# Optimization experiments

Measured on AMD Instinct MI355X. Metric: run time of the kernel, lower is better.

The kernel has to match this reference:

```python
import jax, jax.numpy as jnp
import numpy as np

B, S, D = 2, 2048, 1024
H = 16
HD = D // H  # 64


def setup_inputs() -> dict:
    key = jax.random.key(0)
    ks = jax.random.split(key, 6)
    std = 1.0 / np.sqrt(D)
    x = jax.random.normal(ks[0], (B, S, D), dtype=jnp.float32)
    Wq = jax.random.uniform(ks[1], (D, D), jnp.float32, -std, std)
    Wk = jax.random.uniform(ks[2], (D, D), jnp.float32, -std, std)
    Wv = jax.random.uniform(ks[3], (D, D), jnp.float32, -std, std)
    Wo = jax.random.uniform(ks[4], (D, D), jnp.float32, -std, std)
    bo = jax.random.uniform(ks[5], (D,), jnp.float32, -std, std)
    return {"x": x, "Wq": Wq, "Wk": Wk, "Wv": Wv, "Wo": Wo, "bo": bo}


def reference(x, Wq, Wk, Wv, Wo, bo):
    b, n, _ = x.shape
    # project and split heads: [b, H, n, HD]
    def split_heads(y):
        return y.reshape(b, n, H, HD).transpose(0, 2, 1, 3)
    q = split_heads(jnp.einsum('bnd,ed->bne', x, Wq))
    k = split_heads(jnp.einsum('bnd,ed->bne', x, Wk))
    v = split_heads(jnp.einsum('bnd,ed->bne', x, Wv))
    scores = jnp.einsum('bhqd,bhkd->bhqk', q, k)
    causal = jnp.triu(jnp.ones((n, n), dtype=bool), k=1)
    # original masks with -inf BEFORE scaling; -inf/scale == -inf so math matches
    scores = jnp.where(causal, -jnp.inf, scores) / jnp.sqrt(jnp.asarray(HD, scores.dtype))
    attn = jax.nn.softmax(scores, axis=-1)
    ctx = jnp.einsum('bhqk,bhkd->bhqd', attn, v)
    ctx = ctx.transpose(0, 2, 1, 3).reshape(b, n, D)
    return jnp.einsum('bnd,ed->bne', ctx, Wo) + bo
```

## Files before the change

### kernel.cpp

```cpp
#include <hip/hip_runtime.h>

#define DEV __device__ __forceinline__

typedef __bf16 bf16x8 __attribute__((ext_vector_type(8)));
typedef float f32x4 __attribute__((ext_vector_type(4)));
typedef float f32x16 __attribute__((ext_vector_type(16)));
typedef unsigned u32x4 __attribute__((ext_vector_type(4)));

constexpr int S_LEN = 2048;
constexpr int DMODEL = 1024;
constexpr int NHEAD = 16;
constexpr int HDIM = 64;
constexpr int BATCH = 2;
constexpr int MROWS = BATCH * S_LEN;
constexpr float QSCALE = 0.125f * 1.44269504088896f;

DEV short f2bf(float x) {
  unsigned u = __builtin_bit_cast(unsigned, x);
  unsigned r = u + 0x7fffu + ((u >> 16) & 1u);
  return (short)(r >> 16);
}

#define MFMA16(a, b, c) __builtin_amdgcn_mfma_f32_16x16x32_bf16((a), (b), (c), 0, 0, 0)
#define MFMA32(a, b, c) __builtin_amdgcn_mfma_f32_32x32x16_bf16((a), (b), (c), 0, 0, 0)
#define GLL16(g, l)                                                                     \
  __builtin_amdgcn_global_load_lds((const __attribute__((address_space(1))) void*)(g),  \
                                   (__attribute__((address_space(3))) void*)(l), 16, 0, 0)

DEV unsigned cvt_pk_bf16(float a, float b) {
  unsigned r;
  asm("v_cvt_pk_bf16_f32 %0, %1, %2" : "=v"(r) : "v"(a), "v"(b));
  return r;
}
DEV void swap32(unsigned& a, unsigned& b) {
  asm("v_permlane32_swap_b32 %0, %1" : "+v"(a), "+v"(b));
}

__global__ void cvt_kernel(const float* __restrict__ in, short* __restrict__ out, int n) {
  int i = (blockIdx.x * blockDim.x + threadIdx.x) * 4;
  const int stride = gridDim.x * blockDim.x * 4;
  for (; i < n; i += stride) {
    float4 v = *(const float4*)&in[i];
    short4 r;
    r.x = f2bf(v.x);
    r.y = f2bf(v.y);
    r.z = f2bf(v.z);
    r.w = f2bf(v.w);
    *(short4*)&out[i] = r;
  }
}

__global__ void cvt_w4(const float* __restrict__ Wq, const float* __restrict__ Wk,
                       const float* __restrict__ Wv, const float* __restrict__ Wo,
                       short* __restrict__ out) {
  const float* src = blockIdx.y == 0 ? Wq : blockIdx.y == 1 ? Wk : blockIdx.y == 2 ? Wv : Wo;
  short* dst = out + (size_t)blockIdx.y * (DMODEL * DMODEL);
  int i = (blockIdx.x * blockDim.x + threadIdx.x) * 4;
  const int stride = gridDim.x * blockDim.x * 4;
  for (; i < DMODEL * DMODEL; i += stride) {
    float4 v = *(const float4*)&src[i];
    short4 r;
    r.x = f2bf(v.x);
    r.y = f2bf(v.y);
    r.z = f2bf(v.z);
    r.w = f2bf(v.w);
    *(short4*)&dst[i] = r;
  }
}

__global__ __launch_bounds__(256) void gemm_bt(const short* __restrict__ A,
                                               const short* __restrict__ Bt,
                                               short* __restrict__ outb,
                                               float* __restrict__ outf,
                                               const float* __restrict__ bias,
                                               const int mode) {
  constexpr int K = DMODEL;
  constexpr int N = DMODEL;
  constexpr size_t XN = (size_t)MROWS * DMODEL;
  __shared__ short As[128 * 32];
  __shared__ short Bs[128 * 32];
  const int tid = threadIdx.x;
  const int w = tid >> 6, l = tid & 63;
  const int lr = l & 15, lh = l >> 4;
  const int wr = w >> 1, wc = w & 1;
  const int tm = blockIdx.x, tn = blockIdx.y;

  f32x4 acc[4][4] = {};

  for (int kt = 0; kt < K / 32; ++kt) {
#pragma unroll
    for (int r = 0; r < 2; ++r) {
      const int c = r * 256 + tid;
      const int row = c >> 2;
      const int kc = (c & 3) * 8;
      GLL16(A + (size_t)(tm * 128 + row) * K + kt * 32 + kc, &As[(r * 256 + w * 64) * 8]);
      GLL16(Bt + (size_t)(tn * 128 + row) * K + kt * 32 + kc, &Bs[(r * 256 + w * 64) * 8]);
    }
    __syncthreads();
    bf16x8 af[4], bfr[4];
#pragma unroll
    for (int mi = 0; mi < 4; ++mi)
      af[mi] = *(const bf16x8*)&As[(wr * 64 + mi * 16 + lr) * 32 + lh * 8];
#pragma unroll
    for (int ni = 0; ni < 4; ++ni)
      bfr[ni] = *(const bf16x8*)&Bs[(wc * 64 + ni * 16 + lr) * 32 + lh * 8];
#pragma unroll
    for (int mi = 0; mi < 4; ++mi)
#pragma unroll
      for (int ni = 0; ni < 4; ++ni)
        acc[mi][ni] = MFMA16(af[mi], bfr[ni], acc[mi][ni]);
    __syncthreads();
  }

  const int m0 = tm * 128 + wr * 64;
  const int n0 = tn * 128 + wc * 64;
  if (mode == 3) {
#pragma unroll
    for (int mi = 0; mi < 4; ++mi)
#pragma unroll
      for (int ni = 0; ni < 4; ++ni)
#pragma unroll
        for (int i = 0; i < 4; ++i) {
          const int m = m0 + mi * 16 + lh * 4 + i;
          const int e = n0 + ni * 16 + lr;
          outf[(size_t)m * N + e] = acc[mi][ni][i] + bias[e];
        }
  } else {
    const int sel = tn >> 3;
#pragma unroll
    for (int mi = 0; mi < 4; ++mi)
#pragma unroll
      for (int ni = 0; ni < 4; ++ni)
#pragma unroll
        for (int i = 0; i < 4; ++i) {
          const int m = m0 + mi * 16 + lh * 4 + i;
          const int e = n0 + ni * 16 + lr;
          const int ecol = e & (DMODEL - 1);
          const int b = m >> 11, n = m & (S_LEN - 1);
          const int h = ecol >> 6, d = ecol & (HDIM - 1);
          if (sel == 0)
            outb[((size_t)((b * NHEAD + h) * S_LEN + n)) * HDIM + d] =
                f2bf(acc[mi][ni][i] * QSCALE);
          else if (sel == 1)
            (outb + XN)[((size_t)((b * NHEAD + h) * S_LEN + n)) * HDIM + d] =
                f2bf(acc[mi][ni][i]);
          else
            (outb + 2 * XN)[((size_t)((b * NHEAD + h) * HDIM + d)) * S_LEN + n] =
                f2bf(acc[mi][ni][i]);
        }
  }
}

__global__ __launch_bounds__(256) void attn_kernel(const short* __restrict__ Qg,
                                                   const short* __restrict__ Kg,
                                                   const short* __restrict__ Vg,
                                                   short* __restrict__ ctx) {
  __shared__ alignas(16) short KV[4][8192];
  __shared__ float mls[4][32];
  const int tidx = threadIdx.x;
  const int s = tidx >> 6;
  const int l = tidx & 63;
  const int lq = l & 31;
  const int h5 = l >> 5;
  const int bid = blockIdx.x;
  const int xcd = bid & 7;
  const int j = bid >> 3;
  const int bh = xcd * 4 + (j >> 6);
  const int qi = 63 - (j & 63);
  const int qbase = qi * 32;
  const short* Qh = Qg + (size_t)bh * (S_LEN * HDIM);
  const short* Kh = Kg + (size_t)bh * (S_LEN * HDIM);
  const short* Vh = Vg + (size_t)bh * (HDIM * S_LEN);

  short* Kbase = &KV[s][0];
  short* Vbase = &KV[s][4096];
  const int r8 = l >> 3;
  const int sc = l & 7;

  bf16x8 qf[4];
#pragma unroll
  for (int cc = 0; cc < 4; ++cc)
    qf[cc] = *(const bf16x8*)&Qh[(size_t)(qbase + lq) * HDIM + cc * 16 + h5 * 8];

  f32x16 o0 = {}, o1 = {};
  float ll = 0.f;

  const int ntot = qi + 1;
  const int ts = (ntot * s) >> 2;
  const int te = (ntot * (s + 1)) >> 2;

#define STAGE(T, BUF)                                                              \
  {                                                                                \
    _Pragma("unroll") for (int i = 0; i < 4; ++i) {                                \
      const int R = i * 8 + r8;                                 \
      const int sg = sc ^ (R & 7);          \
      GLL16(Kh + (size_t)((T)*32 + R) * HDIM + sg * 8,                             \
            &Kbase[(BUF)*2048 + i * 512]);                                         \
      GLL16(Vh + (size_t)(2 * R + (sg >> 2)) * S_LEN + (T)*32 + (sg & 3) * 8,      \
            &Vbase[(BUF)*2048 + i * 512]);                                         \
    }                                                                              \
  }

  if (ts < te) STAGE(ts, 0);

  for (int t = ts; t < te; ++t) {
    const int buf = (t - ts) & 1;
    if (t + 1 < te) {
      STAGE(t + 1, buf ^ 1);
      asm volatile("s_waitcnt vmcnt(8)" ::: "memory");
    } else {
      asm volatile("s_waitcnt vmcnt(0)" ::: "memory");
    }
    const short* Ksb = &Kbase[buf * 2048];
    const short* Vsb = &Vbase[buf * 2048];

    bf16x8 kf[4];
#pragma unroll
    for (int cc = 0; cc < 4; ++cc)
      kf[cc] = *(const bf16x8*)&Ksb[lq * 64 + 8 * ((cc * 2 + h5) ^ (lq & 7))];
    f32x16 st = {};
    __builtin_amdgcn_s_setprio(1);
#pragma unroll
    for (int cc = 0; cc < 4; ++cc) st = MFMA32(kf[cc], qf[cc], st);
    __builtin_amdgcn_s_setprio(0);

    if (t == qi) {
#pragma unroll
      for (int rr = 0; rr < 16; ++rr) {
        const int crow = (rr & 3) + 8 * (rr >> 2) + 4 * h5;
        if (crow > lq) st[rr] = -__builtin_inff();
      }
    }

#pragma unroll
    for (int rr = 0; rr < 16; ++rr) {
      st[rr] = __builtin_amdgcn_exp2f(st[rr]);
      ll += st[rr];
    }

    unsigned a0 = cvt_pk_bf16(st[0], st[1]), b0 = cvt_pk_bf16(st[4], st[5]);
    unsigned a1 = cvt_pk_bf16(st[2], st[3]), b1 = cvt_pk_bf16(st[6], st[7]);
    unsigned a2 = cvt_pk_bf16(st[8], st[9]), b2 = cvt_pk_bf16(st[12], st[13]);
    unsigned a3 = cvt_pk_bf16(st[10], st[11]), b3 = cvt_pk_bf16(st[14], st[15]);
    swap32(a0, b0);
    swap32(a1, b1);
    swap32(a2, b2);
    swap32(a3, b3);
    const u32x4 pw0 = {a0, a1, b0, b1};
    const u32x4 pw1 = {a2, a3, b2, b3};
    const bf16x8 pa0 = __builtin_bit_cast(bf16x8, pw0);
    const bf16x8 pa1 = __builtin_bit_cast(bf16x8, pw1);

    const int R0 = lq >> 1, p0 = (lq & 1) * 4 + h5;
    const int R1 = 16 + (lq >> 1);
    const bf16x8 v00 = *(const bf16x8*)&Vsb[R0 * 64 + 8 * ((p0 + 0) ^ (R0 & 7))];
    const bf16x8 v01 = *(const bf16x8*)&Vsb[R0 * 64 + 8 * ((p0 + 2) ^ (R0 & 7))];
    const bf16x8 v10 = *(const bf16x8*)&Vsb[R1 * 64 + 8 * ((p0 + 0) ^ (R1 & 7))];
    const bf16x8 v11 = *(const bf16x8*)&Vsb[R1 * 64 + 8 * ((p0 + 2) ^ (R1 & 7))];
    __builtin_amdgcn_s_setprio(1);
    o0 = MFMA32(pa0, v00, o0);
    o1 = MFMA32(pa0, v10, o1);
    o0 = MFMA32(pa1, v01, o0);
    o1 = MFMA32(pa1, v11, o1);
    __builtin_amdgcn_s_setprio(0);
  }
#undef STAGE

  float* me = (float*)&KV[s][0];
#pragma unroll
  for (int rr = 0; rr < 16; ++rr) {
    const int crow = (rr & 3) + 8 * (rr >> 2) + 4 * h5;
    me[crow * 64 + lq] = o0[rr];
    me[crow * 64 + 32 + lq] = o1[rr];
  }
  ll += __shfl_xor(ll, 32);
  if (h5 == 0) mls[s][lq] = ll;
  __syncthreads();

  const float* om0 = (const float*)&KV[0][0];
  const float* om1 = (const float*)&KV[1][0];
  const float* om2 = (const float*)&KV[2][0];
  const float* om3 = (const float*)&KV[3][0];
  const int b = bh >> 4, h = bh & (NHEAD - 1);
  const int r2 = tidx >> 3;
  const int d0 = (tidx & 7) * 8;
  const float inv =
      __builtin_amdgcn_rcpf(mls[0][r2] + mls[1][r2] + mls[2][r2] + mls[3][r2]);
  const size_t base = (size_t)(b * S_LEN + qbase + r2) * DMODEL + h * HDIM + d0;
#pragma unroll
  for (int i = 0; i < 8; ++i) {
    const int o = r2 * 64 + d0 + i;
    const float v = (om0[o] + om1[o] + om2[o] + om3[o]) * inv;
    ctx[base + i] = f2bf(v);
  }
}

extern "C" void kernel_launch(void* const* d_in, const int* in_sizes, int n_in,
                              void* d_out, int out_size, void* d_ws, size_t ws_size,
                              hipStream_t stream) {
  const float* x = (const float*)d_in[0];
  const float* Wq = (const float*)d_in[1];
  const float* Wk = (const float*)d_in[2];
  const float* Wv = (const float*)d_in[3];
  const float* Wo = (const float*)d_in[4];
  const float* bo = (const float*)d_in[5];

  const size_t XN = (size_t)MROWS * DMODEL;
  const size_t WN = (size_t)DMODEL * DMODEL;

  short* ws = (short*)d_ws;
  short* xb = ws;
  short* Wqb = xb + XN;
  short* Wob = Wqb + 3 * WN;
  short* Qb = Wob + WN;
  short* Kb = Qb + XN;
  short* Vb = Kb + XN;
  short* ctxb = Vb + XN;
  if (ws_size < (5 * XN + 4 * WN) * sizeof(short)) return;

  cvt_kernel<<<2048, 256, 0, stream>>>(x, xb, (int)XN);
  cvt_w4<<<dim3(256, 4), 256, 0, stream>>>(Wq, Wk, Wv, Wo, Wqb);

  gemm_bt<<<dim3(MROWS / 128, 3 * DMODEL / 128), 256, 0, stream>>>(xb, Wqb, Qb, nullptr,
                                                                   nullptr, 4);

  attn_kernel<<<2048, 256, 0, stream>>>(Qb, Kb, Vb, ctxb);

  gemm_bt<<<dim3(MROWS / 128, DMODEL / 128), 256, 0, stream>>>(ctxb, Wob, nullptr,
                                                               (float*)d_out, bo, 3);
}
```

Measured before the change: 134.4 us.

## Double-buffer GEMM LDS tiles with BK=64 and XOR-swizzled layout

The projection GEMM now uses two LDS buffers, prefetching the next K tile through direct global-to-LDS loads while MFMAs run on the current one. The K step grows from 32 to 64, halving the number of barrier iterations, and an XOR swizzle on 16-byte chunks is meant to reduce LDS bank conflicts on fragment reads. LDS use rises from 16KB to 64KB per block, which may lower occupancy.

```diff
diff --git a/kernel.cpp b/kernel.cpp
--- a/kernel.cpp
+++ b/kernel.cpp
@@ -77,40 +77,66 @@
   constexpr int K = DMODEL;
   constexpr int N = DMODEL;
   constexpr size_t XN = (size_t)MROWS * DMODEL;
-  __shared__ short As[128 * 32];
-  __shared__ short Bs[128 * 32];
+  __shared__ short As[2][128 * 64];
+  __shared__ short Bs[2][128 * 64];
   const int tid = threadIdx.x;
   const int w = tid >> 6, l = tid & 63;
   const int lr = l & 15, lh = l >> 4;
   const int wr = w >> 1, wc = w & 1;
   const int tm = blockIdx.x, tn = blockIdx.y;
 
+  const int srow = tid >> 3;
+  const int ssl = tid & 7;
+  const int ssg = ssl ^ (srow & 7);
+
   f32x4 acc[4][4] = {};
 
-  for (int kt = 0; kt < K / 32; ++kt) {
-#pragma unroll
-    for (int r = 0; r < 2; ++r) {
-      const int c = r * 256 + tid;
-      const int row = c >> 2;
-      const int kc = (c & 3) * 8;
-      GLL16(A + (size_t)(tm * 128 + row) * K + kt * 32 + kc, &As[(r * 256 + w * 64) * 8]);
-      GLL16(Bt + (size_t)(tn * 128 + row) * K + kt * 32 + kc, &Bs[(r * 256 + w * 64) * 8]);
+#define GSTAGE(KT, BUF)                                                             \
+  {                                                                                 \
+    _Pragma("unroll") for (int i = 0; i < 4; ++i) {                                 \
+      const int row = i * 32 + srow;                                                \
+      GLL16(A + (size_t)(tm * 128 + row) * K + (KT)*64 + ssg * 8,                   \
+            &As[BUF][(i * 256 + w * 64) * 8]);                                      \
+    }                                                                               \
+    _Pragma("unroll") for (int i = 0; i < 4; ++i) {                                 \
+      const int row = i * 32 + srow;                                                \
+      GLL16(Bt + (size_t)(tn * 128 + row) * K + (KT)*64 + ssg * 8,                  \
+            &Bs[BUF][(i * 256 + w * 64) * 8]);                                      \
+    }                                                                               \
+  }
+
+  GSTAGE(0, 0);
+  asm volatile("s_waitcnt vmcnt(0)" ::: "memory");
+  __syncthreads();
+
+  for (int kt = 0; kt < K / 64; ++kt) {
+    const int buf = kt & 1;
+    if (kt < K / 64 - 1) GSTAGE(kt + 1, buf ^ 1);
+
+#pragma unroll
+    for (int kh = 0; kh < 2; ++kh) {
+      bf16x8 af[4], bfr[4];
+#pragma unroll
+      for (int mi = 0; mi < 4; ++mi) {
+        const int row = wr * 64 + mi * 16 + lr;
+        af[mi] = *(const bf16x8*)&As[buf][row * 64 + 8 * ((kh * 4 + lh) ^ (row & 7))];
+      }
+#pragma unroll
+      for (int ni = 0; ni < 4; ++ni) {
+        const int row = wc * 64 + ni * 16 + lr;
+        bfr[ni] = *(const bf16x8*)&Bs[buf][row * 64 + 8 * ((kh * 4 + lh) ^ (row & 7))];
+      }
+#pragma unroll
+      for (int mi = 0; mi < 4; ++mi)
+#pragma unroll
+        for (int ni = 0; ni < 4; ++ni)
+          acc[mi][ni] = MFMA16(af[mi], bfr[ni], acc[mi][ni]);
     }
+
+    asm volatile("s_waitcnt vmcnt(0)" ::: "memory");
     __syncthreads();
-    bf16x8 af[4], bfr[4];
-#pragma unroll
-    for (int mi = 0; mi < 4; ++mi)
-      af[mi] = *(const bf16x8*)&As[(wr * 64 + mi * 16 + lr) * 32 + lh * 8];
-#pragma unroll
-    for (int ni = 0; ni < 4; ++ni)
-      bfr[ni] = *(const bf16x8*)&Bs[(wc * 64 + ni * 16 + lr) * 32 + lh * 8];
-#pragma unroll
-    for (int mi = 0; mi < 4; ++mi)
-#pragma unroll
-      for (int ni = 0; ni < 4; ++ni)
-        acc[mi][ni] = MFMA16(af[mi], bfr[ni], acc[mi][ni]);
-    __syncthreads();
-  }
+  }
+#undef GSTAGE
 
   const int m0 = tm * 128 + wr * 64;
   const int n0 = tn * 128 + wc * 64;
```

New measurement: 132.5 us. No clear change (-1.4%).

## Double-buffer GEMM LDS tiles, swizzle LDS, and swap MFMA operands for V output

Applied to the files above, without the earlier changes.

The projection GEMM now uses two LDS buffers per operand. The next K tile is prefetched with async global-to-LDS loads while the current tile is consumed, and explicit vmcnt waits plus raw barriers replace the two __syncthreads per step. A row-dependent XOR swizzle on the 16-byte groups is meant to reduce LDS bank conflicts on fragment reads. For mode 4 with V-projection column tiles, the MFMA operands are swapped so each lane holds consecutive sequence positions, making the transposed V store contiguous. The V branch in the generic path is removed, so correctness depends on the host launching the QKV projection with mode 4.

```diff
diff --git a/kernel.cpp b/kernel.cpp
--- a/kernel.cpp
+++ b/kernel.cpp
@@ -76,41 +76,72 @@
                                                const int mode) {
   constexpr int K = DMODEL;
   constexpr int N = DMODEL;
+  constexpr int KT_N = K / 32;
   constexpr size_t XN = (size_t)MROWS * DMODEL;
-  __shared__ short As[128 * 32];
-  __shared__ short Bs[128 * 32];
+  __shared__ short As[2][128 * 32];
+  __shared__ short Bs[2][128 * 32];
   const int tid = threadIdx.x;
   const int w = tid >> 6, l = tid & 63;
   const int lr = l & 15, lh = l >> 4;
   const int wr = w >> 1, wc = w & 1;
   const int tm = blockIdx.x, tn = blockIdx.y;
+  const bool vswap = (mode == 4) && (tn >= 16);
 
   f32x4 acc[4][4] = {};
 
-  for (int kt = 0; kt < K / 32; ++kt) {
-#pragma unroll
-    for (int r = 0; r < 2; ++r) {
-      const int c = r * 256 + tid;
-      const int row = c >> 2;
-      const int kc = (c & 3) * 8;
-      GLL16(A + (size_t)(tm * 128 + row) * K + kt * 32 + kc, &As[(r * 256 + w * 64) * 8]);
-      GLL16(Bt + (size_t)(tn * 128 + row) * K + kt * 32 + kc, &Bs[(r * 256 + w * 64) * 8]);
-    }
-    __syncthreads();
+#define GSTAGE(KT, BUF)                                                      \
+  {                                                                          \
+    _Pragma("unroll") for (int r = 0; r < 2; ++r) {                          \
+      const int c = r * 256 + tid;                         \
+      const int row = c >> 2;                                                \
+      const int g = (c & 3) ^ ((row >> 1) & 3);     \
+      GLL16(A + (size_t)(tm * 128 + row) * K + (KT)*32 + g * 8,              \
+            &As[BUF][(r * 256 + w * 64) * 8]);                               \
+      GLL16(Bt + (size_t)(tn * 128 + row) * K + (KT)*32 + g * 8,             \
+            &Bs[BUF][(r * 256 + w * 64) * 8]);                               \
+    }                                                                        \
+  }
+
+  GSTAGE(0, 0);
+
+  for (int kt = 0; kt < KT_N; ++kt) {
+    const int buf = kt & 1;
+    if (kt + 1 < KT_N) {
+      GSTAGE(kt + 1, buf ^ 1);
+      asm volatile("s_waitcnt vmcnt(4)" ::: "memory");
+    } else {
+      asm volatile("s_waitcnt vmcnt(0)" ::: "memory");
+    }
+    __builtin_amdgcn_s_barrier();
+
     bf16x8 af[4], bfr[4];
 #pragma unroll
-    for (int mi = 0; mi < 4; ++mi)
-      af[mi] = *(const bf16x8*)&As[(wr * 64 + mi * 16 + lr) * 32 + lh * 8];
-#pragma unroll
-    for (int ni = 0; ni < 4; ++ni)
-      bfr[ni] = *(const bf16x8*)&Bs[(wc * 64 + ni * 16 + lr) * 32 + lh * 8];
-#pragma unroll
-    for (int mi = 0; mi < 4; ++mi)
-#pragma unroll
-      for (int ni = 0; ni < 4; ++ni)
-        acc[mi][ni] = MFMA16(af[mi], bfr[ni], acc[mi][ni]);
-    __syncthreads();
-  }
+    for (int mi = 0; mi < 4; ++mi) {
+      const int row = wr * 64 + mi * 16 + lr;
+      af[mi] = *(const bf16x8*)&As[buf][row * 32 + 8 * (lh ^ ((row >> 1) & 3))];
+    }
+#pragma unroll
+    for (int ni = 0; ni < 4; ++ni) {
+      const int row = wc * 64 + ni * 16 + lr;
+      bfr[ni] = *(const bf16x8*)&Bs[buf][row * 32 + 8 * (lh ^ ((row >> 1) & 3))];
+    }
+    if (vswap) {
+#pragma unroll
+      for (int mi = 0; mi < 4; ++mi)
+#pragma unroll
+        for (int ni = 0; ni < 4; ++ni)
+          acc[mi][ni] = MFMA16(bfr[ni], af[mi], acc[mi][ni]);
+    } else {
+#pragma unroll
+      for (int mi = 0; mi < 4; ++mi)
+#pragma unroll
+        for (int ni = 0; ni < 4; ++ni)
+          acc[mi][ni] = MFMA16(af[mi], bfr[ni], acc[mi][ni]);
+    }
+
+    __builtin_amdgcn_s_barrier();
+  }
+#undef GSTAGE
 
   const int m0 = tm * 128 + wr * 64;
   const int n0 = tn * 128 + wc * 64;
@@ -124,6 +155,21 @@
           const int m = m0 + mi * 16 + lh * 4 + i;
           const int e = n0 + ni * 16 + lr;
           outf[(size_t)m * N + e] = acc[mi][ni][i] + bias[e];
+        }
+  } else if (vswap) {
+#pragma unroll
+    for (int mi = 0; mi < 4; ++mi)
+#pragma unroll
+      for (int ni = 0; ni < 4; ++ni)
+#pragma unroll
+        for (int i = 0; i < 4; ++i) {
+          const int e = n0 + ni * 16 + lh * 4 + i;
+          const int m = m0 + mi * 16 + lr;
+          const int ecol = e & (DMODEL - 1);
+          const int b = m >> 11, n = m & (S_LEN - 1);
+          const int h = ecol >> 6, d = ecol & (HDIM - 1);
+          (outb + 2 * XN)[((size_t)((b * NHEAD + h) * HDIM + d)) * S_LEN + n] =
+              f2bf(acc[mi][ni][i]);
         }
   } else {
     const int sel = tn >> 3;
@@ -141,11 +187,8 @@
           if (sel == 0)
             outb[((size_t)((b * NHEAD + h) * S_LEN + n)) * HDIM + d] =
                 f2bf(acc[mi][ni][i] * QSCALE);
-          else if (sel == 1)
+          else
             (outb + XN)[((size_t)((b * NHEAD + h) * S_LEN + n)) * HDIM + d] =
-                f2bf(acc[mi][ni][i]);
-          else
-            (outb + 2 * XN)[((size_t)((b * NHEAD + h) * HDIM + d)) * S_LEN + n] =
                 f2bf(acc[mi][ni][i]);
         }
   }
@@ -192,8 +235,8 @@
 #define STAGE(T, BUF)                                                              \
   {                                                                                \
     _Pragma("unroll") for (int i = 0; i < 4; ++i) {                                \
-      const int R = i * 8 + r8;                                 \
-      const int sg = sc ^ (R & 7);          \
+      const int R = i * 8 + r8;                                                    \
+      const int sg = sc ^ (R & 7);                                                 \
       GLL16(Kh + (size_t)((T)*32 + R) * HDIM + sg * 8,                             \
             &Kbase[(BUF)*2048 + i * 512]);                                         \
       GLL16(Vh + (size_t)(2 * R + (sg >> 2)) * S_LEN + (T)*32 + (sg & 3) * 8,      \
```

After: 137.7 us. 2.4% more time.
